# Optimization experiments

Measured on AMD Instinct MI355X. Metric: run time of the kernel, lower is better.

## Reference

```python
import jax, jax.numpy as jnp
import numpy as np

B, E, C, Fdim, T = 8, 36, 4, 32, 2048
EDGE_DIM, NODE_DIM, NUM_NODES, NUM_CLASSES = 64, 128, 12, 9
# edges: all (i, j) with i in 0..5, j in 6..11, in loop order
U = np.repeat(np.arange(6), 6)
V = np.tile(np.arange(6, 12), 6)


def _p(key, shape, scale=0.05):
    return jax.random.normal(key, shape, jnp.float32) * scale


def setup_inputs():
    ks = iter(jax.random.split(jax.random.key(0), 64))
    nxt = lambda: next(ks)
    inp = {}
    inp["x"] = jax.random.normal(nxt(), (B, E, C, Fdim, T), jnp.float32)
    inp["conv1_w"] = _p(nxt(), (16, C, 3, 3)); inp["conv1_b"] = _p(nxt(), (16,))
    inp["bn1_s"] = jnp.ones((16,)); inp["bn1_b"] = jnp.zeros((16,))
    inp["bn1_m"] = jnp.zeros((16,)); inp["bn1_v"] = jnp.ones((16,))
    inp["se1_w1"] = _p(nxt(), (4, 16)); inp["se1_b1"] = _p(nxt(), (4,))
    inp["se1_w2"] = _p(nxt(), (16, 4)); inp["se1_b2"] = _p(nxt(), (16,))
    inp["conv2_w"] = _p(nxt(), (32, 16, 3, 3)); inp["conv2_b"] = _p(nxt(), (32,))
    inp["bn2_s"] = jnp.ones((32,)); inp["bn2_b"] = jnp.zeros((32,))
    inp["bn2_m"] = jnp.zeros((32,)); inp["bn2_v"] = jnp.ones((32,))
    inp["se2_w1"] = _p(nxt(), (8, 32)); inp["se2_b1"] = _p(nxt(), (8,))
    inp["se2_w2"] = _p(nxt(), (32, 8)); inp["se2_b2"] = _p(nxt(), (32,))
    inp["conv3_w"] = _p(nxt(), (64, 32, 3, 3)); inp["conv3_b"] = _p(nxt(), (64,))
    inp["bn3_s"] = jnp.ones((64,)); inp["bn3_b"] = jnp.zeros((64,))
    inp["bn3_m"] = jnp.zeros((64,)); inp["bn3_v"] = jnp.ones((64,))
    inp["edge_fc_w"] = _p(nxt(), (EDGE_DIM, 64)); inp["edge_fc_b"] = _p(nxt(), (EDGE_DIM,))
    inp["edge_w"] = _p(nxt(), (E,), 1.0)  # learnable_edge_weights
    inp["e2n_w"] = _p(nxt(), (NODE_DIM, EDGE_DIM)); inp["e2n_b"] = _p(nxt(), (NODE_DIM,))
    inp["attn1_w"] = _p(nxt(), (NODE_DIM // 2, NODE_DIM)); inp["attn1_b"] = _p(nxt(), (NODE_DIM // 2,))
    inp["attn2_w"] = _p(nxt(), (1, NODE_DIM // 2))
    inp["cls_w"] = _p(nxt(), (NUM_CLASSES, NODE_DIM)); inp["cls_b"] = _p(nxt(), (NUM_CLASSES,))
    inp["reg_w"] = _p(nxt(), (3, NODE_DIM)); inp["reg_b"] = _p(nxt(), (3,))
    return inp


def _conv(x, w, b, stride):
    y = jax.lax.conv_general_dilated(x, w, window_strides=stride,
        padding=[(1, 1), (1, 1)], dimension_numbers=("NCHW", "OIHW", "NCHW"))
    return y + b[None, :, None, None]


def _bn(x, s, b, m, v):
    # eval-mode BatchNorm2d (running stats)
    inv = s * jax.lax.rsqrt(v + 1e-5)
    return (x - m[None, :, None, None]) * inv[None, :, None, None] + b[None, :, None, None]


def _maxpool2(x):
    return jax.lax.reduce_window(x, -jnp.inf, jax.lax.max,
        (1, 1, 2, 2), (1, 1, 2, 2), "VALID")


def _se(x, w1, b1, w2, b2):
    y = x.mean(axis=(2, 3))                      # [N, C]
    y = jax.nn.relu(y @ w1.T + b1)
    y = jax.nn.sigmoid(y @ w2.T + b2)
    return x * y[:, :, None, None]


def _forward(x, conv1_w, conv1_b, bn1_s, bn1_b, bn1_m, bn1_v,
             se1_w1, se1_b1, se1_w2, se1_b2,
             conv2_w, conv2_b, bn2_s, bn2_b, bn2_m, bn2_v,
             se2_w1, se2_b1, se2_w2, se2_b2,
             conv3_w, conv3_b, bn3_s, bn3_b, bn3_m, bn3_v,
             edge_fc_w, edge_fc_b, edge_w, e2n_w, e2n_b,
             attn1_w, attn1_b, attn2_w, cls_w, cls_b, reg_w, reg_b):
    h = x.reshape(B * E, C, Fdim, T)
    h = jax.nn.relu(_bn(_conv(h, conv1_w, conv1_b, (1, 2)), bn1_s, bn1_b, bn1_m, bn1_v))
    h = _se(_maxpool2(h), se1_w1, se1_b1, se1_w2, se1_b2)
    h = jax.nn.relu(_bn(_conv(h, conv2_w, conv2_b, (1, 2)), bn2_s, bn2_b, bn2_m, bn2_v))
    h = _se(_maxpool2(h), se2_w1, se2_b1, se2_w2, se2_b2)
    h = jax.nn.relu(_bn(_conv(h, conv3_w, conv3_b, (1, 2)), bn3_s, bn3_b, bn3_m, bn3_v))
    h = h.mean(axis=(2, 3))                      # AdaptiveAvgPool2d(1) -> [B*E, 64]
    edge_feat = jax.nn.relu(h @ edge_fc_w.T + edge_fc_b).reshape(B, E, EDGE_DIM)

    # spatial GNN: weighted edge feats scatter-added to both endpoints
    w = jax.nn.softplus(edge_w)[None, :, None]   # [1, E, 1]
    wef = edge_feat * w                          # [B, E, D]
    node = jnp.zeros((B, NUM_NODES, EDGE_DIM), edge_feat.dtype)
    node = node.at[:, U].add(wef).at[:, V].add(wef)
    node = jax.nn.relu(node @ e2n_w.T + e2n_b)   # [B, 12, NODE_DIM]

    # attention pooling
    scores = jnp.tanh(node @ attn1_w.T + attn1_b) @ attn2_w.T   # [B, 12, 1]
    aw = jax.nn.softmax(scores, axis=1)
    ea = aw[:, U, 0] * aw[:, V, 0]               # [B, E]
    ea = ea / (ea.sum(axis=1, keepdims=True) + 1e-8)
    g = (node * aw).sum(axis=1)                  # [B, NODE_DIM]
    return (g @ reg_w.T + reg_b, g @ cls_w.T + cls_b, ea)


def reference(x, conv1_w, conv1_b, bn1_s, bn1_b, bn1_m, bn1_v,
              se1_w1, se1_b1, se1_w2, se1_b2,
              conv2_w, conv2_b, bn2_s, bn2_b, bn2_m, bn2_v,
              se2_w1, se2_b1, se2_w2, se2_b2,
              conv3_w, conv3_b, bn3_s, bn3_b, bn3_m, bn3_v,
              edge_fc_w, edge_fc_b, edge_w, e2n_w, e2n_b,
              attn1_w, attn1_b, attn2_w, cls_w, cls_b, reg_w, reg_b):
    return _forward(x, conv1_w, conv1_b, bn1_s, bn1_b, bn1_m, bn1_v,
                    se1_w1, se1_b1, se1_w2, se1_b2,
                    conv2_w, conv2_b, bn2_s, bn2_b, bn2_m, bn2_v,
                    se2_w1, se2_b1, se2_w2, se2_b2,
                    conv3_w, conv3_b, bn3_s, bn3_b, bn3_m, bn3_v,
                    edge_fc_w, edge_fc_b, edge_w, e2n_w, e2n_b,
                    attn1_w, attn1_b, attn2_w, cls_w, cls_b, reg_w, reg_b)
```

## Files before the change

kernel.cpp:

```cpp
#include <hip/hip_runtime.h>
#include <math.h>


#define GLOAD_LDS(src, dst) \
  __builtin_amdgcn_global_load_lds( \
      (const __attribute__((address_space(1))) void*)(src), \
      (__attribute__((address_space(3))) void*)(dst), 16, 0, 0)

__global__ __launch_bounds__(512) void k_conv1(
    const float* __restrict__ x, const float* __restrict__ w,
    const float* __restrict__ cb, const float* __restrict__ bs,
    const float* __restrict__ bb, const float* __restrict__ bm,
    const float* __restrict__ bv,
    float* __restrict__ h1, float* __restrict__ sesum)
{
  int bid = blockIdx.x;
  int colq = bid & 3, chunk = (bid >> 2) & 3, n = bid >> 4;
  __shared__ float tile[4][6][520];
  __shared__ float wl[4][3][3][16];
  __shared__ float bi[16];

  const float* xn = x + (size_t)n * 4 * 32 * 2048;
  const int cbase = colq * 512;
  for (int i = threadIdx.x; i < 576; i += 512) {
    int co = i / 36, r = i % 36, ci = r / 9, kk = r % 9;
    float s = bs[co] * rsqrtf(bv[co] + 1e-5f);
    wl[ci][kk / 3][kk % 3][co] = w[i] * s;
  }
  if (threadIdx.x < 16) {
    int c = threadIdx.x;
    float s = bs[c] * rsqrtf(bv[c] + 1e-5f);
    bi[c] = bb[c] + (cb[c] - bm[c]) * s;
  }
  int wv = threadIdx.x >> 6, l = threadIdx.x & 63;
  const int P0 = chunk * 4;
  {
    int rowidx = wv & 3;
    int ih = 2 * P0 - 1 + rowidx;
    int slot = ((ih % 6) + 6) % 6;
    int ihc = min(max(ih, 0), 31);
#pragma unroll
    for (int h = 0; h < 2; h++) {
      int ci = (wv >> 2) + 2 * h;
      const float* src = xn + ((size_t)ci * 32 + ihc) * 2048 + cbase + 4 * l;
      GLOAD_LDS(src, &tile[ci][slot][4 + 4 * l]);
      GLOAD_LDS(src + 256, &tile[ci][slot][260 + 4 * l]);
    }
    if (threadIdx.x < 16) {
      int ri = threadIdx.x & 3, ci = threadIdx.x >> 2;
      int ih2 = 2 * P0 - 1 + ri, slot2 = ((ih2 % 6) + 6) % 6;
      int ihc2 = min(max(ih2, 0), 31);
      tile[ci][slot2][3] =
          colq ? xn[((size_t)ci * 32 + ihc2) * 2048 + cbase - 1] : 0.f;
    }
  }
  __syncthreads();

  int cog = threadIdx.x >> 7, tl = threadIdx.x & 127;
  int cob = cog * 4;
  float sloc[4] = {0.f, 0.f, 0.f, 0.f};

#pragma unroll 1
  for (int pl = 0; pl < 4; pl++) {
    int p = P0 + pl;
    if (pl < 3) {
      int rsel = wv & 1, ci = wv >> 1;
      int ih = 2 * p + 3 + rsel;
      int slot = ih % 6;
      int ihc = min(ih, 31);
      const float* src = xn + ((size_t)ci * 32 + ihc) * 2048 + cbase + 4 * l;
      GLOAD_LDS(src, &tile[ci][slot][4 + 4 * l]);
      GLOAD_LDS(src + 256, &tile[ci][slot][260 + 4 * l]);
      if (threadIdx.x < 8) {
        int rs2 = threadIdx.x & 1, ci2 = threadIdx.x >> 1;
        int ih2 = 2 * p + 3 + rs2, slot2 = ih2 % 6, ihc2 = min(ih2, 31);
        tile[ci2][slot2][3] =
            colq ? xn[((size_t)ci2 * 32 + ihc2) * 2048 + cbase - 1] : 0.f;
      }
    }
    float acc[2][2][4];
#pragma unroll
    for (int cr = 0; cr < 2; cr++)
#pragma unroll
      for (int cc = 0; cc < 2; cc++)
#pragma unroll
        for (int k = 0; k < 4; k++) acc[cr][cc][k] = 0.f;
    const bool ok0 = (p > 0), ok3 = (p < 15);
    int slots[4];
#pragma unroll
    for (int r = 0; r < 4; r++) {
      int ih = 2 * p - 1 + r;
      slots[r] = ((ih % 6) + 6) % 6;
    }
#pragma unroll 1
    for (int ci = 0; ci < 4; ci++) {
      float strip[4][5];
#pragma unroll
      for (int r = 0; r < 4; r++) {
        bool ok = (r == 0) ? ok0 : ((r == 3) ? ok3 : true);
        if (ok) {
          float4 vA = *reinterpret_cast<const float4*>(&tile[ci][slots[r]][4 * tl]);
          float4 vB = *reinterpret_cast<const float4*>(&tile[ci][slots[r]][4 * tl + 4]);
          strip[r][0] = vA.w;
          strip[r][1] = vB.x; strip[r][2] = vB.y; strip[r][3] = vB.z; strip[r][4] = vB.w;
        } else {
          strip[r][0] = strip[r][1] = strip[r][2] = strip[r][3] = strip[r][4] = 0.f;
        }
      }
#pragma unroll
      for (int kh = 0; kh < 3; kh++) {
#pragma unroll
        for (int kw = 0; kw < 3; kw++) {
          float4 wv4 = *reinterpret_cast<const float4*>(&wl[ci][kh][kw][cob]);
          float wr[4] = {wv4.x, wv4.y, wv4.z, wv4.w};
#pragma unroll
          for (int cr = 0; cr < 2; cr++) {
            float v0 = strip[cr + kh][kw], v1 = strip[cr + kh][2 + kw];
#pragma unroll
            for (int k = 0; k < 4; k++) {
              acc[cr][0][k] = fmaf(v0, wr[k], acc[cr][0][k]);
              acc[cr][1][k] = fmaf(v1, wr[k], acc[cr][1][k]);
            }
          }
        }
      }
    }
    int pc = colq * 128 + tl;
#pragma unroll
    for (int k = 0; k < 4; k++) {
      float m = fmaxf(fmaxf(acc[0][0][k], acc[0][1][k]),
                      fmaxf(acc[1][0][k], acc[1][1][k]));
      float po = fmaxf(m + bi[cob + k], 0.f);
      h1[(((size_t)n * 16 + cob + k) * 16 + p) * 512 + pc] = po;
      sloc[k] += po;
    }
    __syncthreads();
  }
#pragma unroll
  for (int k = 0; k < 4; k++) {
    float v = sloc[k];
    for (int off = 32; off; off >>= 1) v += __shfl_down(v, off);
    if (l == 0) atomicAdd(&sesum[n * 16 + cob + k], v);
  }
}

__global__ void k_se(const float* __restrict__ sesum, int C, int Cr, float invcnt,
                     const float* __restrict__ w1, const float* __restrict__ b1,
                     const float* __restrict__ w2, const float* __restrict__ b2,
                     float* __restrict__ s)
{
  int n = blockIdx.x * blockDim.x + threadIdx.x;
  if (n >= 288) return;
  float y[32], t[8];
  for (int c = 0; c < C; c++) y[c] = sesum[n * C + c] * invcnt;
  for (int r = 0; r < Cr; r++) {
    float a = b1[r];
    for (int c = 0; c < C; c++) a += y[c] * w1[r * C + c];
    t[r] = fmaxf(a, 0.f);
  }
  for (int c = 0; c < C; c++) {
    float a = b2[c];
    for (int r = 0; r < Cr; r++) a += t[r] * w2[c * Cr + r];
    s[n * C + c] = 1.f / (1.f + expf(-a));
  }
}

__global__ __launch_bounds__(512) void k_conv2(
    const float* __restrict__ h1, const float* __restrict__ w,
    const float* __restrict__ cb, const float* __restrict__ bs,
    const float* __restrict__ bb, const float* __restrict__ bm,
    const float* __restrict__ bv,
    const float* __restrict__ s1,
    float* __restrict__ h2, float* __restrict__ sesum)
{
  int bid = blockIdx.x;
  int ph = bid & 7, n = bid >> 3;
  __shared__ float tile[2][2][4][520];
  __shared__ float wl[16][3][3][32];
  __shared__ float bi[32];

  const float* s1n = s1 + n * 16;
  for (int i = threadIdx.x; i < 4608; i += 512) {
    int co = i / 144, r = i % 144, ci = r / 9, kk = r % 9;
    float s = bs[co] * rsqrtf(bv[co] + 1e-5f);
    wl[ci][kk / 3][kk % 3][co] = w[i] * s * s1n[ci];
  }
  if (threadIdx.x < 32) {
    int c = threadIdx.x;
    float s = bs[c] * rsqrtf(bv[c] + 1e-5f);
    bi[c] = bb[c] + (cb[c] - bm[c]) * s;
  }
  if (threadIdx.x < 64) {
    int b = threadIdx.x >> 5, ci = (threadIdx.x >> 4) & 1,
        r = (threadIdx.x >> 2) & 3, k = threadIdx.x & 3;
    tile[b][ci][r][k] = 0.f;
  }

  const float* hn = h1 + (size_t)n * 16 * 16 * 512;
  int wv = threadIdx.x >> 6, l = threadIdx.x & 63;

  auto stage = [&](int c, int b) {
#pragma unroll
    for (int j = 0; j < 2; j++) {
      int idx = 2 * wv + j;
      int ci_l = idx >> 3, r = (idx >> 1) & 3, half = idx & 1;
      int ci = 2 * c + ci_l;
      int ih = min(max(2 * ph - 1 + r, 0), 15);
      const float* src = hn + ((size_t)ci * 16 + ih) * 512 + half * 256 + 4 * l;
      GLOAD_LDS(src, &tile[b][ci_l][r][4 + half * 256 + 4 * l]);
    }
  };

  stage(0, 0);
  __syncthreads();

  int cog = threadIdx.x >> 7, tl = threadIdx.x & 127;
  int cob = cog * 8;
  const bool ok0 = (ph > 0), ok3 = (ph < 7);
  float acc[2][2][8];
#pragma unroll
  for (int cr = 0; cr < 2; cr++)
#pragma unroll
    for (int cc = 0; cc < 2; cc++)
#pragma unroll
      for (int k = 0; k < 8; k++) acc[cr][cc][k] = 0.f;

#pragma unroll 1
  for (int c = 0; c < 8; c++) {
    if (c < 7) stage(c + 1, (c + 1) & 1);
    const int b = c & 1;
#pragma unroll 1
    for (int ci_l = 0; ci_l < 2; ci_l++) {
      int cg = 2 * c + ci_l;
      float strip[4][5];
#pragma unroll
      for (int r = 0; r < 4; r++) {
        bool ok = (r == 0) ? ok0 : ((r == 3) ? ok3 : true);
        if (ok) {
          float4 vB = *reinterpret_cast<const float4*>(&tile[b][ci_l][r][4 * tl + 4]);
          float4 vA = *reinterpret_cast<const float4*>(&tile[b][ci_l][r][4 * tl]);
          strip[r][0] = vA.w;
          strip[r][1] = vB.x; strip[r][2] = vB.y; strip[r][3] = vB.z; strip[r][4] = vB.w;
        } else {
          strip[r][0] = strip[r][1] = strip[r][2] = strip[r][3] = strip[r][4] = 0.f;
        }
      }
#pragma unroll
      for (int kh = 0; kh < 3; kh++) {
#pragma unroll
        for (int kw = 0; kw < 3; kw++) {
          const float4* wp = reinterpret_cast<const float4*>(&wl[cg][kh][kw][cob]);
          float4 w0 = wp[0], w1 = wp[1];
          float wr[8] = {w0.x, w0.y, w0.z, w0.w, w1.x, w1.y, w1.z, w1.w};
#pragma unroll
          for (int cr = 0; cr < 2; cr++) {
            float v0 = strip[cr + kh][kw], v1 = strip[cr + kh][2 + kw];
#pragma unroll
            for (int k = 0; k < 8; k++) {
              acc[cr][0][k] = fmaf(v0, wr[k], acc[cr][0][k]);
              acc[cr][1][k] = fmaf(v1, wr[k], acc[cr][1][k]);
            }
          }
        }
      }
    }
    if (c < 7) __syncthreads();
  }

#pragma unroll
  for (int k = 0; k < 8; k++) {
    float m = fmaxf(fmaxf(acc[0][0][k], acc[0][1][k]),
                    fmaxf(acc[1][0][k], acc[1][1][k]));
    float po = fmaxf(m + bi[cob + k], 0.f);
    h2[(((size_t)n * 32 + cob + k) * 8 + ph) * 128 + tl] = po;
    float v = po;
    for (int off = 32; off; off >>= 1) v += __shfl_down(v, off);
    if (l == 0) atomicAdd(&sesum[n * 32 + cob + k], v);
  }
}

__global__ __launch_bounds__(256) void k_conv3(
    const float* __restrict__ h2, const float* __restrict__ w,
    const float* __restrict__ cb, const float* __restrict__ bs,
    const float* __restrict__ bb, const float* __restrict__ bm,
    const float* __restrict__ bv,
    const float* __restrict__ s2, float* __restrict__ h3)
{
  int bid = blockIdx.x;
  int n = bid >> 2, cog = bid & 3;
  int hh = threadIdx.x >> 5, t = threadIdx.x & 31;
  __shared__ float tile[8][8][128];
  __shared__ float wl[32][3][3][16];
  __shared__ float bi[16];
  __shared__ float red[4][16];
  const float* s2n = s2 + n * 32;
  for (int i = threadIdx.x; i < 4608; i += 256) {
    int k = i / 288, r = i % 288, ci = r / 9, kk = r % 9;
    int co = cog * 16 + k;
    float s = bs[co] * rsqrtf(bv[co] + 1e-5f);
    wl[ci][kk / 3][kk % 3][k] = w[(size_t)co * 288 + r] * s * s2n[ci];
  }
  if (threadIdx.x < 16) {
    int c = cog * 16 + threadIdx.x;
    float s = bs[c] * rsqrtf(bv[c] + 1e-5f);
    bi[threadIdx.x] = bb[c] + (cb[c] - bm[c]) * s;
  }
  const float* hn = h2 + (size_t)n * 32 * 8 * 128;
  int wv = threadIdx.x >> 6, l = threadIdx.x & 63;
  const int aoff = t ? 4 * t - 4 : 0;
  float acc[2][16];
#pragma unroll
  for (int cc = 0; cc < 2; cc++)
#pragma unroll
    for (int k = 0; k < 16; k++) acc[cc][k] = 0.f;

#pragma unroll 1
  for (int c = 0; c < 4; c++) {
    for (int i = 0; i < 8; i++) {
      int pair = wv * 8 + i;
      int ci_l = pair >> 2, r2 = (pair & 3) * 2;
      int ci = c * 8 + ci_l;
      const float* src = hn + ((size_t)ci * 8 + r2) * 128 + 4 * l;
      GLOAD_LDS(src, &tile[ci_l][r2][4 * l]);
    }
    __syncthreads();
#pragma unroll 1
    for (int ci_l = 0; ci_l < 8; ci_l++) {
      int cg = c * 8 + ci_l;
      float strip[3][5];
#pragma unroll
      for (int r = 0; r < 3; r++) {
        int ih = hh - 1 + r;
        if (ih >= 0 && ih <= 7) {
          float4 vB = *reinterpret_cast<const float4*>(&tile[ci_l][ih][4 * t]);
          float4 vA = *reinterpret_cast<const float4*>(&tile[ci_l][ih][aoff]);
          strip[r][0] = t ? vA.w : 0.f;
          strip[r][1] = vB.x; strip[r][2] = vB.y; strip[r][3] = vB.z; strip[r][4] = vB.w;
        } else {
          strip[r][0] = strip[r][1] = strip[r][2] = strip[r][3] = strip[r][4] = 0.f;
        }
      }
#pragma unroll
      for (int kh = 0; kh < 3; kh++) {
#pragma unroll
        for (int kw = 0; kw < 3; kw++) {
          const float4* wp = reinterpret_cast<const float4*>(&wl[cg][kh][kw][0]);
          float4 w0 = wp[0], w1 = wp[1], w2 = wp[2], w3 = wp[3];
          float wr[16] = {w0.x, w0.y, w0.z, w0.w, w1.x, w1.y, w1.z, w1.w,
                          w2.x, w2.y, w2.z, w2.w, w3.x, w3.y, w3.z, w3.w};
          float v0 = strip[kh][kw], v1 = strip[kh][2 + kw];
#pragma unroll
          for (int k = 0; k < 16; k++) {
            acc[0][k] = fmaf(v0, wr[k], acc[0][k]);
            acc[1][k] = fmaf(v1, wr[k], acc[1][k]);
          }
        }
      }
    }
    __syncthreads();
  }
#pragma unroll
  for (int k = 0; k < 16; k++)
    acc[0][k] = fmaxf(acc[0][k] + bi[k], 0.f) + fmaxf(acc[1][k] + bi[k], 0.f);
#pragma unroll
  for (int k = 0; k < 16; k++) {
    float v = acc[0][k];
    for (int off = 32; off; off >>= 1) v += __shfl_down(v, off);
    if (l == 0) red[wv][k] = v;
  }
  __syncthreads();
  if (threadIdx.x < 16) {
    int k = threadIdx.x;
    float tt = red[0][k] + red[1][k] + red[2][k] + red[3][k];
    h3[n * 64 + cog * 16 + k] = tt * (1.f / 512.f);
  }
}

__global__ __launch_bounds__(256) void k_head(
    const float* __restrict__ h3,
    const float* __restrict__ efw, const float* __restrict__ efb,
    const float* __restrict__ ew,
    const float* __restrict__ e2nw, const float* __restrict__ e2nb,
    const float* __restrict__ a1w, const float* __restrict__ a1b,
    const float* __restrict__ a2w,
    const float* __restrict__ clsw, const float* __restrict__ clsb,
    const float* __restrict__ regw, const float* __restrict__ regb,
    float* __restrict__ out)
{
  int b = blockIdx.x;
  int tid = threadIdx.x;
  __shared__ float ef[36][64];
  __shared__ float nin[12][64];
  __shared__ float nd[12][128];
  __shared__ float tmp[12][64];
  __shared__ float spw[36], aw[12], scv[12], g[128], ea[36];
  if (tid < 36) {
    float xw = ew[tid];
    spw[tid] = (xw > 20.f) ? xw : log1pf(expf(xw));
  }
  __syncthreads();
  for (int idx = tid; idx < 36 * 64; idx += 256) {
    int e = idx >> 6, d = idx & 63;
    const float* hr = h3 + (size_t)(b * 36 + e) * 64;
    const float* wr = efw + d * 64;
    float a = efb[d];
    for (int k = 0; k < 64; k++) a += hr[k] * wr[k];
    ef[e][d] = fmaxf(a, 0.f) * spw[e];
  }
  __syncthreads();
  for (int idx = tid; idx < 12 * 64; idx += 256) {
    int j = idx >> 6, d = idx & 63;
    float a = 0.f;
    if (j < 6) { for (int i = 0; i < 6; i++) a += ef[j * 6 + i][d]; }
    else       { for (int i = 0; i < 6; i++) a += ef[i * 6 + (j - 6)][d]; }
    nin[j][d] = a;
  }
  __syncthreads();
  for (int idx = tid; idx < 12 * 128; idx += 256) {
    int j = idx >> 7, d = idx & 127;
    const float* wr = e2nw + d * 64;
    float a = e2nb[d];
    for (int k = 0; k < 64; k++) a += nin[j][k] * wr[k];
    nd[j][d] = fmaxf(a, 0.f);
  }
  __syncthreads();
  for (int idx = tid; idx < 12 * 64; idx += 256) {
    int j = idx >> 6, hh = idx & 63;
    const float* wr = a1w + hh * 128;
    float a = a1b[hh];
    for (int k = 0; k < 128; k++) a += nd[j][k] * wr[k];
    tmp[j][hh] = tanhf(a) * a2w[hh];
  }
  __syncthreads();
  if (tid < 12) {
    float a = 0.f;
    for (int h = 0; h < 64; h++) a += tmp[tid][h];
    scv[tid] = a;
  }
  __syncthreads();
  if (tid == 0) {
    float m = scv[0];
    for (int j = 1; j < 12; j++) m = fmaxf(m, scv[j]);
    float s = 0.f;
    for (int j = 0; j < 12; j++) { float z = expf(scv[j] - m); aw[j] = z; s += z; }
    float inv = 1.f / s;
    for (int j = 0; j < 12; j++) aw[j] *= inv;
    float rs = 0.f;
    for (int e = 0; e < 36; e++) { float r = aw[e / 6] * aw[6 + e % 6]; ea[e] = r; rs += r; }
    float inv2 = 1.f / (rs + 1e-8f);
    for (int e = 0; e < 36; e++) ea[e] *= inv2;
  }
  __syncthreads();
  if (tid < 36) out[96 + b * 36 + tid] = ea[tid];
  if (tid < 128) {
    float a = 0.f;
    for (int j = 0; j < 12; j++) a += nd[j][tid] * aw[j];
    g[tid] = a;
  }
  __syncthreads();
  if (tid < 3) {
    const float* wr = regw + tid * 128;
    float a = regb[tid];
    for (int k = 0; k < 128; k++) a += g[k] * wr[k];
    out[b * 3 + tid] = a;
  }
  if (tid >= 64 && tid < 73) {
    int i = tid - 64;
    const float* wr = clsw + i * 128;
    float a = clsb[i];
    for (int k = 0; k < 128; k++) a += g[k] * wr[k];
    out[24 + b * 9 + i] = a;
  }
}

extern "C" void kernel_launch(void* const* d_in, const int* in_sizes, int n_in,
                              void* d_out, int out_size, void* d_ws, size_t ws_size,
                              hipStream_t stream) {
  const float* x      = (const float*)d_in[0];
  const float* c1w    = (const float*)d_in[1];
  const float* c1b    = (const float*)d_in[2];
  const float* bn1s   = (const float*)d_in[3];
  const float* bn1b   = (const float*)d_in[4];
  const float* bn1m   = (const float*)d_in[5];
  const float* bn1v   = (const float*)d_in[6];
  const float* se1w1  = (const float*)d_in[7];
  const float* se1b1  = (const float*)d_in[8];
  const float* se1w2  = (const float*)d_in[9];
  const float* se1b2  = (const float*)d_in[10];
  const float* c2w    = (const float*)d_in[11];
  const float* c2b    = (const float*)d_in[12];
  const float* bn2s   = (const float*)d_in[13];
  const float* bn2b   = (const float*)d_in[14];
  const float* bn2m   = (const float*)d_in[15];
  const float* bn2v   = (const float*)d_in[16];
  const float* se2w1  = (const float*)d_in[17];
  const float* se2b1  = (const float*)d_in[18];
  const float* se2w2  = (const float*)d_in[19];
  const float* se2b2  = (const float*)d_in[20];
  const float* c3w    = (const float*)d_in[21];
  const float* c3b    = (const float*)d_in[22];
  const float* bn3s   = (const float*)d_in[23];
  const float* bn3b   = (const float*)d_in[24];
  const float* bn3m   = (const float*)d_in[25];
  const float* bn3v   = (const float*)d_in[26];
  const float* efw    = (const float*)d_in[27];
  const float* efb    = (const float*)d_in[28];
  const float* ew     = (const float*)d_in[29];
  const float* e2nw   = (const float*)d_in[30];
  const float* e2nb   = (const float*)d_in[31];
  const float* a1w    = (const float*)d_in[32];
  const float* a1b    = (const float*)d_in[33];
  const float* a2w    = (const float*)d_in[34];
  const float* clsw   = (const float*)d_in[35];
  const float* clsb   = (const float*)d_in[36];
  const float* regw   = (const float*)d_in[37];
  const float* regb   = (const float*)d_in[38];

  float* ws = (float*)d_ws;
  float* h1     = ws;
  float* h2     = h1 + 37748736;
  float* sesum1 = h2 + 9437184;
  float* s1     = sesum1 + 4608;
  float* sesum2 = s1 + 4608;
  float* s2     = sesum2 + 9216;
  float* h3     = s2 + 9216;

  hipMemsetAsync(sesum1, 0, 4608 * sizeof(float), stream);
  hipMemsetAsync(sesum2, 0, 9216 * sizeof(float), stream);

  k_conv1<<<288 * 16, 512, 0, stream>>>(x, c1w, c1b, bn1s, bn1b, bn1m, bn1v, h1, sesum1);
  k_se<<<5, 64, 0, stream>>>(sesum1, 16, 4, 1.f / 8192.f, se1w1, se1b1, se1w2, se1b2, s1);
  k_conv2<<<288 * 8, 512, 0, stream>>>(h1, c2w, c2b, bn2s, bn2b, bn2m, bn2v, s1, h2, sesum2);
  k_se<<<5, 64, 0, stream>>>(sesum2, 32, 8, 1.f / 1024.f, se2w1, se2b1, se2w2, se2b2, s2);
  k_conv3<<<288 * 4, 256, 0, stream>>>(h2, c3w, c3b, bn3s, bn3b, bn3m, bn3v, s2, h3);
  k_head<<<8, 256, 0, stream>>>(h3, efw, efb, ew, e2nw, e2nb, a1w, a1b, a2w,
                                clsw, clsb, regw, regb, (float*)d_out);
}
```

Measured before the change: 586.5 us.

## Retile conv1 into full-height 64-column tiles with single-shot load

Conv1 is retiled so each block loads all 32 input rows for a 64-column strip of every channel in one shot into LDS, with a separate halo array for the left column. This replaces the rolling 6-row ring buffer with per-pooled-row syncs. Each thread now computes 8 output channels instead of 4, for one pooled row and one column pair. The aim is to remove the per-row barriers and serialized load/compute loop and to reuse weights across more channels per thread. In exchange it doubles the grid size, increases register pressure, and loads less data per block.

```diff
diff --git a/kernel.cpp b/kernel.cpp
--- a/kernel.cpp
+++ b/kernel.cpp
@@ -9,138 +9,114 @@
 
 __global__ __launch_bounds__(512) void k_conv1(
     const float* __restrict__ x, const float* __restrict__ w,
-    const float* __restrict__ cb, const float* __restrict__ bs,
+    const float* __restrict__ cb_, const float* __restrict__ bs,
     const float* __restrict__ bb, const float* __restrict__ bm,
     const float* __restrict__ bv,
     float* __restrict__ h1, float* __restrict__ sesum)
 {
   int bid = blockIdx.x;
-  int colq = bid & 3, chunk = (bid >> 2) & 3, n = bid >> 4;
-  __shared__ float tile[4][6][520];
+  int cb = bid & 31, n = bid >> 5;
+  __shared__ float tile[4][32][64];
+  __shared__ float halo[4][32];
   __shared__ float wl[4][3][3][16];
   __shared__ float bi[16];
 
   const float* xn = x + (size_t)n * 4 * 32 * 2048;
-  const int cbase = colq * 512;
-  for (int i = threadIdx.x; i < 576; i += 512) {
+  const int cbase = cb * 64;
+  int tid = threadIdx.x;
+  for (int i = tid; i < 576; i += 512) {
     int co = i / 36, r = i % 36, ci = r / 9, kk = r % 9;
     float s = bs[co] * rsqrtf(bv[co] + 1e-5f);
     wl[ci][kk / 3][kk % 3][co] = w[i] * s;
   }
-  if (threadIdx.x < 16) {
-    int c = threadIdx.x;
+  if (tid < 16) {
+    int c = tid;
     float s = bs[c] * rsqrtf(bv[c] + 1e-5f);
-    bi[c] = bb[c] + (cb[c] - bm[c]) * s;
-  }
-  int wv = threadIdx.x >> 6, l = threadIdx.x & 63;
-  const int P0 = chunk * 4;
-  {
-    int rowidx = wv & 3;
-    int ih = 2 * P0 - 1 + rowidx;
-    int slot = ((ih % 6) + 6) % 6;
-    int ihc = min(max(ih, 0), 31);
-#pragma unroll
-    for (int h = 0; h < 2; h++) {
-      int ci = (wv >> 2) + 2 * h;
-      const float* src = xn + ((size_t)ci * 32 + ihc) * 2048 + cbase + 4 * l;
-      GLOAD_LDS(src, &tile[ci][slot][4 + 4 * l]);
-      GLOAD_LDS(src + 256, &tile[ci][slot][260 + 4 * l]);
+    bi[c] = bb[c] + (cb_[c] - bm[c]) * s;
+  }
+  if (tid >= 128 && tid < 256) {
+    int t2 = tid - 128;
+    int ci = t2 >> 5, r = t2 & 31;
+    halo[ci][r] = cb ? xn[((size_t)ci * 32 + r) * 2048 + cbase - 1] : 0.f;
+  }
+  int wv = tid >> 6, l = tid & 63;
+#pragma unroll
+  for (int j = 0; j < 4; j++) {
+    int idx = wv * 4 + j;
+    int ci = idx >> 3, r4 = (idx & 7) * 4;
+    const float* src =
+        xn + ((size_t)ci * 32 + r4 + (l >> 4)) * 2048 + cbase + (l & 15) * 4;
+    GLOAD_LDS(src, &tile[ci][r4][0] + 4 * l);
+  }
+  __syncthreads();
+
+  int cog = tid >> 8;
+  int ph = (tid >> 4) & 15;
+  int tl = tid & 15;
+  int cob = cog * 8;
+  const int r0 = 2 * ph - 1;
+
+  float acc[2][2][8];
+#pragma unroll
+  for (int cr = 0; cr < 2; cr++)
+#pragma unroll
+    for (int cc = 0; cc < 2; cc++)
+#pragma unroll
+      for (int k = 0; k < 8; k++) acc[cr][cc][k] = 0.f;
+
+#pragma unroll 1
+  for (int ci = 0; ci < 4; ci++) {
+    float strip[4][5];
+#pragma unroll
+    for (int r = 0; r < 4; r++) {
+      int ir = r0 + r;
+      bool ok = (ir >= 0) && (ir <= 31);
+      int irc = min(max(ir, 0), 31);
+      const float* rowp = &tile[ci][irc][0];
+      float4 vB = *reinterpret_cast<const float4*>(rowp + 4 * tl);
+      float4 vA = *reinterpret_cast<const float4*>(rowp + (tl ? 4 * tl - 4 : 0));
+      float h0 = tl ? vA.w : halo[ci][irc];
+      strip[r][0] = ok ? h0 : 0.f;
+      strip[r][1] = ok ? vB.x : 0.f;
+      strip[r][2] = ok ? vB.y : 0.f;
+      strip[r][3] = ok ? vB.z : 0.f;
+      strip[r][4] = ok ? vB.w : 0.f;
     }
-    if (threadIdx.x < 16) {
-      int ri = threadIdx.x & 3, ci = threadIdx.x >> 2;
-      int ih2 = 2 * P0 - 1 + ri, slot2 = ((ih2 % 6) + 6) % 6;
-      int ihc2 = min(max(ih2, 0), 31);
-      tile[ci][slot2][3] =
-          colq ? xn[((size_t)ci * 32 + ihc2) * 2048 + cbase - 1] : 0.f;
-    }
-  }
-  __syncthreads();
-
-  int cog = threadIdx.x >> 7, tl = threadIdx.x & 127;
-  int cob = cog * 4;
-  float sloc[4] = {0.f, 0.f, 0.f, 0.f};
-
-#pragma unroll 1
-  for (int pl = 0; pl < 4; pl++) {
-    int p = P0 + pl;
-    if (pl < 3) {
-      int rsel = wv & 1, ci = wv >> 1;
-      int ih = 2 * p + 3 + rsel;
-      int slot = ih % 6;
-      int ihc = min(ih, 31);
-      const float* src = xn + ((size_t)ci * 32 + ihc) * 2048 + cbase + 4 * l;
-      GLOAD_LDS(src, &tile[ci][slot][4 + 4 * l]);
-      GLOAD_LDS(src + 256, &tile[ci][slot][260 + 4 * l]);
-      if (threadIdx.x < 8) {
-        int rs2 = threadIdx.x & 1, ci2 = threadIdx.x >> 1;
-        int ih2 = 2 * p + 3 + rs2, slot2 = ih2 % 6, ihc2 = min(ih2, 31);
-        tile[ci2][slot2][3] =
-            colq ? xn[((size_t)ci2 * 32 + ihc2) * 2048 + cbase - 1] : 0.f;
-      }
-    }
-    float acc[2][2][4];
-#pragma unroll
-    for (int cr = 0; cr < 2; cr++)
-#pragma unroll
-      for (int cc = 0; cc < 2; cc++)
-#pragma unroll
-        for (int k = 0; k < 4; k++) acc[cr][cc][k] = 0.f;
-    const bool ok0 = (p > 0), ok3 = (p < 15);
-    int slots[4];
-#pragma unroll
-    for (int r = 0; r < 4; r++) {
-      int ih = 2 * p - 1 + r;
-      slots[r] = ((ih % 6) + 6) % 6;
-    }
-#pragma unroll 1
-    for (int ci = 0; ci < 4; ci++) {
-      float strip[4][5];
-#pragma unroll
-      for (int r = 0; r < 4; r++) {
-        bool ok = (r == 0) ? ok0 : ((r == 3) ? ok3 : true);
-        if (ok) {
-          float4 vA = *reinterpret_cast<const float4*>(&tile[ci][slots[r]][4 * tl]);
-          float4 vB = *reinterpret_cast<const float4*>(&tile[ci][slots[r]][4 * tl + 4]);
-          strip[r][0] = vA.w;
-          strip[r][1] = vB.x; strip[r][2] = vB.y; strip[r][3] = vB.z; strip[r][4] = vB.w;
-        } else {
-          strip[r][0] = strip[r][1] = strip[r][2] = strip[r][3] = strip[r][4] = 0.f;
-        }
-      }
-#pragma unroll
-      for (int kh = 0; kh < 3; kh++) {
-#pragma unroll
-        for (int kw = 0; kw < 3; kw++) {
-          float4 wv4 = *reinterpret_cast<const float4*>(&wl[ci][kh][kw][cob]);
-          float wr[4] = {wv4.x, wv4.y, wv4.z, wv4.w};
-#pragma unroll
-          for (int cr = 0; cr < 2; cr++) {
-            float v0 = strip[cr + kh][kw], v1 = strip[cr + kh][2 + kw];
-#pragma unroll
-            for (int k = 0; k < 4; k++) {
-              acc[cr][0][k] = fmaf(v0, wr[k], acc[cr][0][k]);
-              acc[cr][1][k] = fmaf(v1, wr[k], acc[cr][1][k]);
-            }
+#pragma unroll
+    for (int kh = 0; kh < 3; kh++) {
+#pragma unroll
+      for (int kw = 0; kw < 3; kw++) {
+        const float4* wp = reinterpret_cast<const float4*>(&wl[ci][kh][kw][cob]);
+        float4 w0 = wp[0], w1 = wp[1];
+        float wr[8] = {w0.x, w0.y, w0.z, w0.w, w1.x, w1.y, w1.z, w1.w};
+#pragma unroll
+        for (int cr = 0; cr < 2; cr++) {
+          float v0 = strip[cr + kh][kw], v1 = strip[cr + kh][2 + kw];
+#pragma unroll
+          for (int k = 0; k < 8; k++) {
+            acc[cr][0][k] = fmaf(v0, wr[k], acc[cr][0][k]);
+            acc[cr][1][k] = fmaf(v1, wr[k], acc[cr][1][k]);
           }
         }
       }
     }
-    int pc = colq * 128 + tl;
-#pragma unroll
-    for (int k = 0; k < 4; k++) {
-      float m = fmaxf(fmaxf(acc[0][0][k], acc[0][1][k]),
-                      fmaxf(acc[1][0][k], acc[1][1][k]));
-      float po = fmaxf(m + bi[cob + k], 0.f);
-      h1[(((size_t)n * 16 + cob + k) * 16 + p) * 512 + pc] = po;
-      sloc[k] += po;
-    }
-    __syncthreads();
-  }
-#pragma unroll
-  for (int k = 0; k < 4; k++) {
-    float v = sloc[k];
+  }
+
+  int pc = cb * 16 + tl;
+  float pooled[8];
+#pragma unroll
+  for (int k = 0; k < 8; k++) {
+    float m = fmaxf(fmaxf(acc[0][0][k], acc[0][1][k]),
+                    fmaxf(acc[1][0][k], acc[1][1][k]));
+    pooled[k] = fmaxf(m + bi[cob + k], 0.f);
+    h1[(((size_t)n * 16 + cob + k) * 16 + ph) * 512 + pc] = pooled[k];
+  }
+  int lane = tid & 63;
+#pragma unroll
+  for (int k = 0; k < 8; k++) {
+    float v = pooled[k];
     for (int off = 32; off; off >>= 1) v += __shfl_down(v, off);
-    if (l == 0) atomicAdd(&sesum[n * 16 + cob + k], v);
+    if (lane == 0) atomicAdd(&sesum[n * 16 + cob + k], v);
   }
 }
 
@@ -528,7 +504,7 @@
   hipMemsetAsync(sesum1, 0, 4608 * sizeof(float), stream);
   hipMemsetAsync(sesum2, 0, 9216 * sizeof(float), stream);
 
-  k_conv1<<<288 * 16, 512, 0, stream>>>(x, c1w, c1b, bn1s, bn1b, bn1m, bn1v, h1, sesum1);
+  k_conv1<<<288 * 32, 512, 0, stream>>>(x, c1w, c1b, bn1s, bn1b, bn1m, bn1v, h1, sesum1);
   k_se<<<5, 64, 0, stream>>>(sesum1, 16, 4, 1.f / 8192.f, se1w1, se1b1, se1w2, se1b2, s1);
   k_conv2<<<288 * 8, 512, 0, stream>>>(h1, c2w, c2b, bn2s, bn2b, bn2m, bn2v, s1, h2, sesum2);
   k_se<<<5, 64, 0, stream>>>(sesum2, 32, 8, 1.f / 1024.f, se2w1, se2b1, se2w2, se2b2, s2);
```

After: 696.0 us. 1.19x slower.
